# Kernel optimization log

Hardware: AMD Instinct MI355X
Metric: run time of the kernel (lower is better)

## Reference

```python
import jax, jax.numpy as jnp
import numpy as np

# Hard-coded dims from MambaLayer.__init__
D_IN = 20        # input feature dim (Dense infers it; chosen = modelInternalDim)
D_INNER = 20     # modelInternalDim
N_STATES = 10    # modelStates
DT_RANK = 5      # delta_t_rank
BATCH = 4
SEQ = 32768


def setup_inputs() -> dict:
    key = jax.random.key(0)
    ks = jax.random.split(key, 8)
    s = lambda k, shape: jax.random.normal(k, shape, dtype=jnp.float32) * 0.05
    A = jnp.tile(jnp.arange(1, N_STATES + 1, dtype=jnp.float32)[None, :], (D_INNER, 1))
    return {
        "x": jax.random.normal(ks[0], (BATCH, SEQ, D_IN), dtype=jnp.float32),
        "w_in": s(ks[1], (D_IN, 2 * D_INNER)),
        "b_in": jnp.zeros((2 * D_INNER,), jnp.float32),
        "conv_k": s(ks[2], (3, D_INNER, D_INNER)),   # (W, I, O)
        "conv_b": jnp.zeros((D_INNER,), jnp.float32),
        "w_x": s(ks[3], (D_INNER, DT_RANK + 2 * N_STATES)),
        "b_x": jnp.zeros((DT_RANK + 2 * N_STATES,), jnp.float32),
        "w_dt": s(ks[4], (DT_RANK, D_INNER)),
        "b_dt": jnp.zeros((D_INNER,), jnp.float32),
        "A_log": jnp.log(A),
        "D_param": jnp.ones((D_INNER,), jnp.float32),
    }


def _selective_scan(u, delta, A, B, C, D):
    # u, delta: (b,l,d); A: (d,n); B, C: (b,l,n); D: (d,)
    dA = jnp.einsum('bld,dn->bldn', delta, A)                  # (b,l,d,n)
    dB_u = jnp.einsum('bld,bld,bln->bldn', delta, u, B)        # (b,l,d,n)
    # tf.pad(dA[:,1:], [[0,0],[1,1],...])[:,1:] == concat(dA[:,1:], zeros) along l
    dA_shift = jnp.concatenate([dA[:, 1:], jnp.zeros_like(dA[:, :1])], axis=1)
    # reversed cumsum, exponentiate, reverse back
    dA_cumsum = jnp.exp(jnp.flip(jnp.cumsum(jnp.flip(dA_shift, axis=1), axis=1), axis=1))
    x = jnp.cumsum(dB_u * dA_cumsum, axis=1) / (dA_cumsum + 1e-12)
    y = jnp.einsum('bldn,bln->bld', x, C)
    return y + u * D


def reference(x, w_in, b_in, conv_k, conv_b, w_x, b_x, w_dt, b_dt, A_log, D_param):
    # in_projection + split (res half is unused, matching the original call())
    h = x @ w_in + b_in                                        # (b,l,2d)
    h, _res = jnp.split(h, 2, axis=-1)
    # causal Conv1D, kernel_size=3: left-pad by 2
    h = jax.lax.conv_general_dilated(
        h, conv_k, window_strides=(1,), padding=[(2, 0)],
        dimension_numbers=('NWC', 'WIO', 'NWC')) + conv_b
    h = jax.nn.silu(h)                                         # tf.nn.swish
    # ssm
    A = -jnp.exp(A_log)                                        # (d,n)
    xp = h @ w_x + b_x                                         # (b,l,r+2n)
    delta = xp[..., :DT_RANK]
    Bm = xp[..., DT_RANK:DT_RANK + N_STATES]
    Cm = xp[..., DT_RANK + N_STATES:]
    delta = jax.nn.softmax(delta @ w_dt + b_dt, axis=-1)       # (b,l,d)
    return _selective_scan(h, delta, A, Bm, Cm, D_param)
```

## Files before the change

### kernel.cpp

```cpp
#include <hip/hip_runtime.h>
#include <math.h>

#define B_   4
#define L_   32768
#define DI   20
#define NS   10
#define TBLK 128
#define NCB  256

#define OFF_AP   0u
#define OFF_RS   204800u
#define OFF_SC   409600u
#define OFF_TOT  430080u
#define OFF_H16  430192u
#define HD  0u
#define HU  2621440u
#define HB  5242880u
#define HC  6553600u

typedef _Float16 h16;
typedef _Float16 half8 __attribute__((ext_vector_type(8)));
typedef _Float16 half4 __attribute__((ext_vector_type(4)));
typedef float f32x4 __attribute__((ext_vector_type(4)));

template<int CTRL>
__device__ __forceinline__ float dppf(float idv, float src) {
    union U { float f; int i; };
    U o, s, r; o.f = idv; s.f = src;
    r.i = __builtin_amdgcn_update_dpp(o.i, s.i, CTRL, 0xf, 0xf, false);
    return r.f;
}
#define ROW_SHR1 0x111
#define ROW_SHR2 0x112
#define ROW_SHR4 0x114
#define ROW_SHR8 0x118

#define OPSCAN16(Ac, Bc) \
    { float aP = dppf<ROW_SHR1>(1.0f, Ac); float bP = dppf<ROW_SHR1>(0.0f, Bc); \
      Bc = fmaf(Ac, bP, Bc); Ac *= aP; \
      aP = dppf<ROW_SHR2>(1.0f, Ac); bP = dppf<ROW_SHR2>(0.0f, Bc); \
      Bc = fmaf(Ac, bP, Bc); Ac *= aP; \
      aP = dppf<ROW_SHR4>(1.0f, Ac); bP = dppf<ROW_SHR4>(0.0f, Bc); \
      Bc = fmaf(Ac, bP, Bc); Ac *= aP; \
      aP = dppf<ROW_SHR8>(1.0f, Ac); bP = dppf<ROW_SHR8>(0.0f, Bc); \
      Bc = fmaf(Ac, bP, Bc); Ac *= aP; }

#define SUMSCAN16(v) \
    { v += dppf<ROW_SHR1>(0.0f, v); v += dppf<ROW_SHR2>(0.0f, v); \
      v += dppf<ROW_SHR4>(0.0f, v); v += dppf<ROW_SHR8>(0.0f, v); }

#define XS_   0
#define MT_   2640
#define UL_   0
#define DS__  0
#define DUS_  2720
#define XP5_  4608
#define BS_   5448
#define WXo   6808
#define WDTo  7808
#define BDTo  7908
#define BXo   7928
#define POOLH 7956
#define WF_   7956
#define POOL2 (POOLH + 3200)

__global__ __launch_bounds__(320) void k1(
    const float* __restrict__ x,
    const float* __restrict__ w_in, const float* __restrict__ b_in,
    const float* __restrict__ conv_k, const float* __restrict__ conv_b,
    const float* __restrict__ w_x, const float* __restrict__ b_x,
    const float* __restrict__ w_dt, const float* __restrict__ b_dt,
    const float* __restrict__ A_log, const float* __restrict__ D_param,
    h16* __restrict__ dh, h16* __restrict__ uh,
    h16* __restrict__ Bh, h16* __restrict__ Ch,
    float* __restrict__ ap_ws, float* __restrict__ rs_ws, float* __restrict__ sc_ws,
    float* __restrict__ out)
{
    __shared__ __align__(16) h16 P[POOL2];
    __shared__ float beff_s[20];
    __shared__ float ALs[200];
    __shared__ float D_s[20];

    const int tid = threadIdx.x;
    const int c   = blockIdx.x;
    const int b   = blockIdx.y;
    const int l0  = c * TBLK;

    {
        float* Wf = (float*)&P[WF_];
        for (int i = tid; i < 400;  i += 320) Wf[i]       = w_in[(i/20)*40 + (i%20)];
        for (int i = tid; i < 1200; i += 320) Wf[400 + i] = conv_k[i];
        for (int i = tid; i < 200;  i += 320) ALs[i] = -__expf(A_log[i]);
        if (tid < 20) D_s[tid] = D_param[tid];
    }
    __syncthreads();

    {
        const float* Wf = (const float*)&P[WF_];
        for (int e = tid; e < 1200; e += 320) {
            int cc = e/20, o = e - cc*20;
            int w = cc/20, i = cc - w*20;
            float acc = 0.0f;
            #pragma unroll
            for (int op = 0; op < 20; op++)
                acc = fmaf(Wf[i*20 + op], Wf[400 + (w*20 + op)*20 + o], acc);
            P[MT_ + o*72 + cc] = (h16)acc;
        }
        for (int i = tid; i < 240; i += 320) {
            int o = i/12, cc = 60 + (i - (i/12)*12);
            P[MT_ + o*72 + cc] = (h16)0.0f;
        }
        for (int i = tid; i < 1000; i += 320) {
            int j = i/40, k = i - j*40;
            P[WXo + i] = (k < 20) ? (h16)w_x[k*25 + j] : (h16)0.0f;
        }
        for (int i = tid; i < 100; i += 320) P[WDTo + i] = (h16)w_dt[i];
        if (tid < 20) P[BDTo + tid] = (h16)b_dt[tid];
        if (tid < 25) P[BXo + tid] = (h16)b_x[tid];
        if (tid < 20) {
            float be = conv_b[tid];
            #pragma unroll
            for (int w = 0; w < 3; w++)
                #pragma unroll
                for (int op = 0; op < 20; op++)
                    be = fmaf(b_in[op], Wf[400 + (w*20 + op)*20 + tid], be);
            beff_s[tid] = be;
        }
        const float* xb = x + ((size_t)b*L_ + l0)*DI - 2*DI;
        for (int i = tid; i < 1320; i += 320) {
            float2 v;
            if (i >= 1300 || (c == 0 && i < 20)) v = make_float2(0.0f, 0.0f);
            else v = *(const float2*)(xb + 2*i);
            P[XS_ + 2*i]     = (h16)v.x;
            P[XS_ + 2*i + 1] = (h16)v.y;
        }
    }
    __syncthreads();

    const int wv  = tid >> 6;
    const int ln  = tid & 63;
    const int m16 = ln & 15;
    const int q   = ln >> 4;
    float uval[4][4];
    if (wv < 4) {
        #pragma unroll
        for (int jj = 0; jj < 4; jj++) {
            int job = wv*4 + jj, mt = job >> 1, nt = job & 1;
            int t_row = mt*16 + m16;
            int dcol  = nt*16 + m16;
            int dmin  = dcol < 20 ? dcol : 19;
            f32x4 acc = {0.0f, 0.0f, 0.0f, 0.0f};
            #pragma unroll
            for (int kh = 0; kh < 2; kh++) {
                half8 af, bf;
                int ab = XS_ + t_row*20 + kh*32 + (q<<3);
                *(half4*)&af         = *(const half4*)&P[ab];
                *(((half4*)&af) + 1) = *(const half4*)&P[ab + 4];
                int bb = MT_ + dmin*72 + kh*32 + (q<<3);
                *(half4*)&bf         = *(const half4*)&P[bb];
                *(((half4*)&bf) + 1) = *(const half4*)&P[bb + 4];
                acc = __builtin_amdgcn_mfma_f32_16x16x32_f16(af, bf, acc, 0, 0, 0);
            }
            float bfv = beff_s[dmin];
            #pragma unroll
            for (int r = 0; r < 4; r++) {
                float a = acc[r] + bfv;
                uval[jj][r] = a * __builtin_amdgcn_rcpf(1.0f + __expf(-a));
            }
        }
    }
    __syncthreads();

    if (wv < 4) {
        #pragma unroll
        for (int jj = 0; jj < 4; jj++) {
            int job = wv*4 + jj, mt = job >> 1, nt = job & 1;
            int dcol = nt*16 + m16;
            if (dcol < 20) {
                #pragma unroll
                for (int r = 0; r < 4; r++)
                    P[UL_ + (mt*16 + q*4 + r)*36 + dcol] = (h16)uval[jj][r];
            }
        }
    }
    __syncthreads();

    float xv[4][4];
    if (wv < 4) {
        #pragma unroll
        for (int jj = 0; jj < 4; jj++) {
            int job = wv*4 + jj, mt = job >> 1, nt = job & 1;
            int t_row = mt*16 + m16;
            int j     = nt*16 + m16;
            int jmin  = j < 25 ? j : 24;
            f32x4 acc = {0.0f, 0.0f, 0.0f, 0.0f};
            half8 af, bf;
            int ab = UL_ + t_row*36 + (q<<3);
            *(half4*)&af         = *(const half4*)&P[ab];
            *(((half4*)&af) + 1) = *(const half4*)&P[ab + 4];
            int bb = WXo + jmin*40 + (q<<3);
            *(half4*)&bf         = *(const half4*)&P[bb];
            *(((half4*)&bf) + 1) = *(const half4*)&P[bb + 4];
            acc = __builtin_amdgcn_mfma_f32_16x16x32_f16(af, bf, acc, 0, 0, 0);
            float bx = (j < 25) ? (float)P[BXo + j] : 0.0f;
            #pragma unroll
            for (int r = 0; r < 4; r++) xv[jj][r] = acc[r] + bx;
        }
        #pragma unroll
        for (int jj = 0; jj < 4; jj++) {
            int job = wv*4 + jj, mt = job >> 1, nt = job & 1;
            int j = nt*16 + m16;
            #pragma unroll
            for (int r = 0; r < 4; r++) {
                int t = mt*16 + q*4 + r;
                h16 hv = (h16)xv[jj][r];
                if (j < 5)       P[XP5_ + t*5 + j] = hv;
                else if (j < 15) P[BS_ + (j - 5)*136 + t] = hv;
                else if (j < 25) Ch[(size_t)(b*NS + (j - 15))*L_ + l0 + t] = hv;
            }
        }
    }
    __syncthreads();

    h16 urow[20];
    float dl[20];
    if (tid < 128) {
        const int t = tid;
        *(half4*)&urow[0]  = *(const half4*)&P[UL_ + t*36 + 0];
        *(half4*)&urow[4]  = *(const half4*)&P[UL_ + t*36 + 4];
        *(half4*)&urow[8]  = *(const half4*)&P[UL_ + t*36 + 8];
        *(half4*)&urow[12] = *(const half4*)&P[UL_ + t*36 + 12];
        *(half4*)&urow[16] = *(const half4*)&P[UL_ + t*36 + 16];
        #pragma unroll
        for (int d2 = 0; d2 < 20; d2++)
            uh[(size_t)(b*DI + d2)*L_ + l0 + t] = urow[d2];
        #pragma unroll
        for (int n = 0; n < NS; n++)
            Bh[(size_t)(b*NS + n)*L_ + l0 + t] = P[BS_ + n*136 + t];
        {
            float yo[20];
            #pragma unroll
            for (int d2 = 0; d2 < 20; d2++) yo[d2] = (float)urow[d2] * D_s[d2];
            float4* ob = (float4*)(out + ((size_t)b*L_ + l0 + t)*DI);
            #pragma unroll
            for (int k4 = 0; k4 < 5; k4++)
                ob[k4] = make_float4(yo[4*k4], yo[4*k4+1], yo[4*k4+2], yo[4*k4+3]);
        }
        float xq[5];
        #pragma unroll
        for (int r = 0; r < 5; r++) xq[r] = (float)P[XP5_ + t*5 + r];
        #pragma unroll
        for (int d2 = 0; d2 < 20; d2++) dl[d2] = (float)P[BDTo + d2];
        #pragma unroll
        for (int r = 0; r < 5; r++) {
            float dv = xq[r];
            #pragma unroll
            for (int d2 = 0; d2 < 20; d2++)
                dl[d2] = fmaf(dv, (float)P[WDTo + r*20 + d2], dl[d2]);
        }
        float mx = dl[0];
        #pragma unroll
        for (int d2 = 1; d2 < 20; d2++) mx = fmaxf(mx, dl[d2]);
        float sm = 0.0f;
        #pragma unroll
        for (int d2 = 0; d2 < 20; d2++) { dl[d2] = __expf(dl[d2] - mx); sm += dl[d2]; }
        float inv = __builtin_amdgcn_rcpf(sm);
        #pragma unroll
        for (int d2 = 0; d2 < 20; d2++) dl[d2] *= inv;
    }
    __syncthreads();

    if (tid < 128) {
        const int t = tid;
        #pragma unroll
        for (int d2 = 0; d2 < 20; d2++) {
            h16 dlh = (h16)dl[d2];
            P[DS__ + d2*136 + t] = dlh;
            P[DUS_ + d2*136 + t] = (h16)((float)dlh * (float)urow[d2]);
            dh[(size_t)(b*DI + d2)*L_ + l0 + t] = dlh;
        }
    }
    __syncthreads();

    const int d  = tid >> 4;
    const int s  = tid & 15;
    const int bd = b*DI + d;

    float d8[8], du8[8];
    { half8 hv = *(const half8*)&P[DS__ + d*136 + 8*s];
      #pragma unroll
      for (int j = 0; j < 8; j++) d8[j] = (float)hv[j]; }
    { half8 hv = *(const half8*)&P[DUS_ + d*136 + 8*s];
      #pragma unroll
      for (int j = 0; j < 8; j++) du8[j] = (float)hv[j]; }

    float loc8 = 0.0f;
    #pragma unroll
    for (int j = 0; j < 8; j++) loc8 += d8[j];
    float ssum = loc8;
    SUMSCAN16(ssum);
    if (s == 15) sc_ws[(size_t)bd*NCB + c] = ssum;

    float A_dn[NS];
    #pragma unroll
    for (int n = 0; n < NS; n++) A_dn[n] = ALs[d*NS + n];

    bool fastA = true;
    #pragma unroll
    for (int n = 1; n < NS; n++)
        fastA = fastA &&
            (fabsf(A_dn[n] - (float)(n+1)*A_dn[0]) <= 1e-3f*fabsf(A_dn[n]) + 1e-6f);

    float AcA[NS], BcA[NS];
    if (fastA) {
        float e1[8], ep[8];
        #pragma unroll
        for (int j = 0; j < 8; j++) { e1[j] = __expf(A_dn[0]*d8[j]); ep[j] = e1[j]; }
        #pragma unroll
        for (int n = 0; n < NS; n++) {
            half8 bv = *(const half8*)&P[BS_ + n*136 + 8*s];
            float Bc = 0.0f;
            #pragma unroll
            for (int j = 0; j < 8; j++)
                Bc = fmaf(ep[j], Bc, du8[j]*(float)bv[j]);
            BcA[n] = Bc;
            AcA[n] = __expf(A_dn[n]*loc8);
            if (n < NS-1) {
                #pragma unroll
                for (int j = 0; j < 8; j++) ep[j] *= e1[j];
            }
        }
    } else {
        #pragma unroll
        for (int n = 0; n < NS; n++) {
            half8 bv = *(const half8*)&P[BS_ + n*136 + 8*s];
            float Bc = 0.0f;
            #pragma unroll
            for (int j = 0; j < 8; j++) {
                float a = __expf(A_dn[n]*d8[j]);
                Bc = fmaf(a, Bc, du8[j]*(float)bv[j]);
            }
            BcA[n] = Bc;
            AcA[n] = __expf(A_dn[n]*loc8);
        }
    }
    #pragma unroll
    for (int n = 0; n < NS; n++) { OPSCAN16(AcA[n], BcA[n]); }
    if (s == 15) {
        const size_t o0 = ((size_t)bd*NS)*NCB + c;
        #pragma unroll
        for (int n = 0; n < NS; n++) {
            ap_ws[o0 + (size_t)n*NCB] = AcA[n];
            rs_ws[o0 + (size_t)n*NCB] = BcA[n];
        }
    }
}

__global__ __launch_bounds__(64) void kC2(
    const float* __restrict__ ap_ws, float* __restrict__ rs_ws,
    float* __restrict__ sc_ws, float* __restrict__ tot_ws)
{
    const int bd   = blockIdx.x;
    const int lane = threadIdx.x;
    const size_t sb = (size_t)bd*NCB + lane*4;

    float4 sv = *(const float4*)(sc_ws + sb);
    float l1 = sv.x, l2 = l1 + sv.y, l3 = l2 + sv.z, l4 = l3 + sv.w;
    float inc = l4;
    #pragma unroll
    for (int off = 1; off < 64; off <<= 1) {
        float t = __shfl_up(inc, off);
        if (lane >= off) inc += t;
    }
    float ex = __shfl_up(inc, 1);
    if (lane == 0) ex = 0.0f;
    *(float4*)(sc_ws + sb) = make_float4(ex, ex + l1, ex + l2, ex + l3);
    if (lane == 63) tot_ws[bd] = inc;

    #pragma unroll 2
    for (int n = 0; n < NS; n++) {
        const size_t base = ((size_t)bd*NS + n)*NCB + lane*4;
        float4 av = *(const float4*)(ap_ws + base);
        float4 rv = *(const float4*)(rs_ws + base);
        float Ac = av.x, Bc = rv.x;
        Bc = fmaf(av.y, Bc, rv.y); Ac *= av.y;
        Bc = fmaf(av.z, Bc, rv.z); Ac *= av.z;
        Bc = fmaf(av.w, Bc, rv.w); Ac *= av.w;
        #pragma unroll
        for (int off = 1; off < 64; off <<= 1) {
            float aP = __shfl_up(Ac, off);
            float bP = __shfl_up(Bc, off);
            if (lane >= off) { Bc = fmaf(Ac, bP, Bc); Ac *= aP; }
        }
        float pB = __shfl_up(Bc, 1);
        if (lane == 0) pB = 0.0f;
        float r  = pB;
        float o0 = r; r = fmaf(av.x, r, rv.x);
        float o1 = r; r = fmaf(av.y, r, rv.y);
        float o2 = r; r = fmaf(av.z, r, rv.z);
        float o3 = r;
        *(float4*)(rs_ws + base) = make_float4(o0, o1, o2, o3);
    }
}

__global__ __launch_bounds__(320) void kD(
    const h16* __restrict__ dh, const h16* __restrict__ uh,
    const h16* __restrict__ Bh, const h16* __restrict__ Ch,
    const float* __restrict__ A_log, const float* __restrict__ D_param,
    const float* __restrict__ rs_ws, const float* __restrict__ sc_ws,
    const float* __restrict__ tot_ws, float* __restrict__ out)
{
    __shared__ float ylT[20*132];
    __shared__ int anyact;
    const int tid = threadIdx.x;
    const int d   = tid >> 4;
    const int s   = tid & 15;
    const int c   = blockIdx.x;
    const int b   = blockIdx.y;
    const int bd  = b*DI + d;
    const size_t t0 = (size_t)c*TBLK + s*8;

    const float Tot = tot_ws[bd];
    float mnlog = A_log[d*NS];
    #pragma unroll
    for (int n = 1; n < NS; n++) mnlog = fminf(mnlog, A_log[d*NS + n]);
    const float Amax = -__expf(mnlog);
    const float pref_end = (c + 1 < NCB) ? sc_ws[(size_t)bd*NCB + c + 1] : Tot;
    const bool active = fmaf(Amax, Tot - pref_end, 40.0f) > 0.0f;

    if (tid == 0) anyact = 0;
    __syncthreads();
    if (active) anyact = 1;
    __syncthreads();
    if (anyact == 0) return;

    float u8[8];
    { half8 hv = *(const half8*)(uh + (size_t)bd*L_ + t0);
      #pragma unroll
      for (int j = 0; j < 8; j++) u8[j] = (float)hv[j]; }
    const float Dd = D_param[d];
    float yv[8];
    #pragma unroll
    for (int j = 0; j < 8; j++) yv[j] = u8[j]*Dd;

    if (active) {
        float A_dn[NS];
        #pragma unroll
        for (int n = 0; n < NS; n++) A_dn[n] = -__expf(A_log[d*NS + n]);
        bool fastA = true;
        #pragma unroll
        for (int n = 1; n < NS; n++)
            fastA = fastA &&
                (fabsf(A_dn[n] - (float)(n+1)*A_dn[0]) <= 1e-3f*fabsf(A_dn[n]) + 1e-6f);

        float d8[8], du8[8];
        { half8 hv = *(const half8*)(dh + (size_t)bd*L_ + t0);
          #pragma unroll
          for (int j = 0; j < 8; j++) d8[j] = (float)hv[j]; }
        #pragma unroll
        for (int j = 0; j < 8; j++) du8[j] = d8[j]*u8[j];

        float lp[8];
        { float run = 0.0f;
          #pragma unroll
          for (int j = 0; j < 8; j++) { run += d8[j]; lp[j] = run; } }
        float inc = lp[7];
        SUMSCAN16(inc);
        float ex = dppf<ROW_SHR1>(0.0f, inc);
        const float basep = sc_ws[(size_t)bd*NCB + c] + ex;

        float rin[NS];
        #pragma unroll
        for (int n = 0; n < NS; n++) rin[n] = rs_ws[((size_t)bd*NS + n)*NCB + c];

        float yacc[8];
        #pragma unroll
        for (int j = 0; j < 8; j++) yacc[j] = 0.0f;

        if (fastA) {
            float e1[8], ep[8];
            #pragma unroll
            for (int j = 0; j < 8; j++) { e1[j] = __expf(A_dn[0]*d8[j]); ep[j] = e1[j]; }
            #pragma unroll
            for (int n = 0; n < NS; n++) {
                half8 bv = *(const half8*)(Bh + (size_t)(b*NS + n)*L_ + t0);
                half8 cv = *(const half8*)(Ch + (size_t)(b*NS + n)*L_ + t0);
                float b8[8];
                #pragma unroll
                for (int j = 0; j < 8; j++) b8[j] = du8[j]*(float)bv[j];
                float Bc = 0.0f;
                #pragma unroll
                for (int j = 0; j < 8; j++) Bc = fmaf(ep[j], Bc, b8[j]);
                float Ac = __expf(A_dn[n]*lp[7]);
                OPSCAN16(Ac, Bc);
                float pA = dppf<ROW_SHR1>(1.0f, Ac);
                float pB = dppf<ROW_SHR1>(0.0f, Bc);
                float r  = fmaf(pA, rin[n], pB);

                float G[8];
                G[7] = __expf(A_dn[n]*(Tot - (basep + lp[7])));
                #pragma unroll
                for (int j = 6; j >= 0; j--) G[j] = G[j+1]*ep[j+1];
                #pragma unroll
                for (int j = 0; j < 8; j++) {
                    r = fmaf(ep[j], r, b8[j]);
                    float damp = G[j] * __builtin_amdgcn_rcpf(G[j] + 1e-12f);
                    yacc[j] = fmaf((float)cv[j]*damp, r, yacc[j]);
                }
                if (n < NS-1) {
                    #pragma unroll
                    for (int j = 0; j < 8; j++) ep[j] *= e1[j];
                }
            }
        } else {
            #pragma unroll 2
            for (int n = 0; n < NS; n++) {
                half8 bv = *(const half8*)(Bh + (size_t)(b*NS + n)*L_ + t0);
                half8 cv = *(const half8*)(Ch + (size_t)(b*NS + n)*L_ + t0);
                float a8[8], b8[8];
                #pragma unroll
                for (int j = 0; j < 8; j++) {
                    a8[j] = __expf(A_dn[n]*d8[j]);
                    b8[j] = du8[j]*(float)bv[j];
                }
                float Bc = 0.0f;
                #pragma unroll
                for (int j = 0; j < 8; j++) Bc = fmaf(a8[j], Bc, b8[j]);
                float Ac = __expf(A_dn[n]*lp[7]);
                OPSCAN16(Ac, Bc);
                float pA = dppf<ROW_SHR1>(1.0f, Ac);
                float pB = dppf<ROW_SHR1>(0.0f, Bc);
                float r  = fmaf(pA, rin[n], pB);

                float G[8];
                G[7] = __expf(A_dn[n]*(Tot - (basep + lp[7])));
                #pragma unroll
                for (int j = 6; j >= 0; j--) G[j] = G[j+1]*a8[j+1];
                #pragma unroll
                for (int j = 0; j < 8; j++) {
                    r = fmaf(a8[j], r, b8[j]);
                    float damp = G[j] * __builtin_amdgcn_rcpf(G[j] + 1e-12f);
                    yacc[j] = fmaf((float)cv[j]*damp, r, yacc[j]);
                }
            }
        }
        #pragma unroll
        for (int j = 0; j < 8; j++) yv[j] = fmaf(u8[j], Dd, yacc[j]);
    }

    *(float4*)&ylT[d*132 + 8*s]     = *(float4*)(yv);
    *(float4*)&ylT[d*132 + 8*s + 4] = *(float4*)(yv + 4);
    __syncthreads();

    float4* ob4 = (float4*)(out + ((size_t)b*L_ + (size_t)c*TBLK)*DI);
    for (int i = tid; i < TBLK*DI/4; i += 320) {
        int t = i / 5, qq = (i - t*5)*4;
        ob4[i] = make_float4(ylT[qq*132 + t], ylT[(qq+1)*132 + t],
                             ylT[(qq+2)*132 + t], ylT[(qq+3)*132 + t]);
    }
}

extern "C" void kernel_launch(void* const* d_in, const int* in_sizes, int n_in,
                              void* d_out, int out_size, void* d_ws, size_t ws_size,
                              hipStream_t stream) {
    const float* x      = (const float*)d_in[0];
    const float* w_in   = (const float*)d_in[1];
    const float* b_in   = (const float*)d_in[2];
    const float* conv_k = (const float*)d_in[3];
    const float* conv_b = (const float*)d_in[4];
    const float* w_x    = (const float*)d_in[5];
    const float* b_x    = (const float*)d_in[6];
    const float* w_dt   = (const float*)d_in[7];
    const float* b_dt   = (const float*)d_in[8];
    const float* A_log  = (const float*)d_in[9];
    const float* D_par  = (const float*)d_in[10];
    float* out = (float*)d_out;
    float* ws  = (float*)d_ws;

    float* ap_ws  = ws + OFF_AP;
    float* rs_ws  = ws + OFF_RS;
    float* sc_ws  = ws + OFF_SC;
    float* tot_ws = ws + OFF_TOT;
    h16*   hbase  = (h16*)(ws + OFF_H16);
    h16* dh  = hbase + HD;
    h16* uh  = hbase + HU;
    h16* Bh  = hbase + HB;
    h16* Ch  = hbase + HC;

    k1<<<dim3(NCB, B_), 320, 0, stream>>>(x, w_in, b_in, conv_k, conv_b,
                                          w_x, b_x, w_dt, b_dt, A_log, D_par,
                                          dh, uh, Bh, Ch,
                                          ap_ws, rs_ws, sc_ws, out);
    kC2<<<B_*DI, 64, 0, stream>>>(ap_ws, rs_ws, sc_ws, tot_ws);
    kD<<<dim3(NCB, B_), 320, 0, stream>>>(dh, uh, Bh, Ch, A_log, D_par,
                                          rs_ws, sc_ws, tot_ws, out);
}
```

Baseline: 117.1 us.

## Fold chunk-carry scan kernel into final kernel, recomputing prefixes per block

Removes the separate kC2 launch that scanned the per-chunk totals and state carries. Each kD block now rereads all 256 chunk summaries for its channel and, with 16 lanes per channel, does a masked reduction and operator scan to get its own prefix total and incoming state. This drops a launch and a device-wide dependency step. In exchange every block does redundant work, roughly quadratic in the chunk count overall, and rereads the ap/rs workspace.

```diff
diff --git a/kernel.cpp b/kernel.cpp
--- a/kernel.cpp
+++ b/kernel.cpp
@@ -11,7 +11,6 @@
 #define OFF_AP   0u
 #define OFF_RS   204800u
 #define OFF_SC   409600u
-#define OFF_TOT  430080u
 #define OFF_H16  430192u
 #define HD  0u
 #define HU  2621440u
@@ -356,76 +355,47 @@
     }
 }
 
-__global__ __launch_bounds__(64) void kC2(
-    const float* __restrict__ ap_ws, float* __restrict__ rs_ws,
-    float* __restrict__ sc_ws, float* __restrict__ tot_ws)
-{
-    const int bd   = blockIdx.x;
-    const int lane = threadIdx.x;
-    const size_t sb = (size_t)bd*NCB + lane*4;
-
-    float4 sv = *(const float4*)(sc_ws + sb);
-    float l1 = sv.x, l2 = l1 + sv.y, l3 = l2 + sv.z, l4 = l3 + sv.w;
-    float inc = l4;
-    #pragma unroll
-    for (int off = 1; off < 64; off <<= 1) {
-        float t = __shfl_up(inc, off);
-        if (lane >= off) inc += t;
-    }
-    float ex = __shfl_up(inc, 1);
-    if (lane == 0) ex = 0.0f;
-    *(float4*)(sc_ws + sb) = make_float4(ex, ex + l1, ex + l2, ex + l3);
-    if (lane == 63) tot_ws[bd] = inc;
-
-    #pragma unroll 2
-    for (int n = 0; n < NS; n++) {
-        const size_t base = ((size_t)bd*NS + n)*NCB + lane*4;
-        float4 av = *(const float4*)(ap_ws + base);
-        float4 rv = *(const float4*)(rs_ws + base);
-        float Ac = av.x, Bc = rv.x;
-        Bc = fmaf(av.y, Bc, rv.y); Ac *= av.y;
-        Bc = fmaf(av.z, Bc, rv.z); Ac *= av.z;
-        Bc = fmaf(av.w, Bc, rv.w); Ac *= av.w;
-        #pragma unroll
-        for (int off = 1; off < 64; off <<= 1) {
-            float aP = __shfl_up(Ac, off);
-            float bP = __shfl_up(Bc, off);
-            if (lane >= off) { Bc = fmaf(Ac, bP, Bc); Ac *= aP; }
-        }
-        float pB = __shfl_up(Bc, 1);
-        if (lane == 0) pB = 0.0f;
-        float r  = pB;
-        float o0 = r; r = fmaf(av.x, r, rv.x);
-        float o1 = r; r = fmaf(av.y, r, rv.y);
-        float o2 = r; r = fmaf(av.z, r, rv.z);
-        float o3 = r;
-        *(float4*)(rs_ws + base) = make_float4(o0, o1, o2, o3);
-    }
-}
-
 __global__ __launch_bounds__(320) void kD(
     const h16* __restrict__ dh, const h16* __restrict__ uh,
     const h16* __restrict__ Bh, const h16* __restrict__ Ch,
     const float* __restrict__ A_log, const float* __restrict__ D_param,
-    const float* __restrict__ rs_ws, const float* __restrict__ sc_ws,
-    const float* __restrict__ tot_ws, float* __restrict__ out)
+    const float* __restrict__ ap_ws, const float* __restrict__ rs_ws,
+    const float* __restrict__ sc_ws, float* __restrict__ out)
 {
     __shared__ float ylT[20*132];
     __shared__ int anyact;
     const int tid = threadIdx.x;
     const int d   = tid >> 4;
     const int s   = tid & 15;
+    const int lnw = tid & 63;
     const int c   = blockIdx.x;
     const int b   = blockIdx.y;
     const int bd  = b*DI + d;
     const size_t t0 = (size_t)c*TBLK + s*8;
 
-    const float Tot = tot_ws[bd];
+    float totp = 0.0f, clipp = 0.0f;
+    {
+        const float4* sc4 = (const float4*)(sc_ws + (size_t)bd*NCB + s*16);
+        #pragma unroll
+        for (int q4 = 0; q4 < 4; q4++) {
+            float4 v = sc4[q4];
+            int base = s*16 + q4*4;
+            totp  += v.x + v.y + v.z + v.w;
+            clipp += (base + 0 < c ? v.x : 0.0f) + (base + 1 < c ? v.y : 0.0f)
+                   + (base + 2 < c ? v.z : 0.0f) + (base + 3 < c ? v.w : 0.0f);
+        }
+    }
+    SUMSCAN16(totp);
+    SUMSCAN16(clipp);
+    const float Tot = __shfl(totp,  lnw | 15);
+    const float Pc  = __shfl(clipp, lnw | 15);
+    const float sc_c = sc_ws[(size_t)bd*NCB + c];
+    const float pref_end = Pc + sc_c;
+
     float mnlog = A_log[d*NS];
     #pragma unroll
     for (int n = 1; n < NS; n++) mnlog = fminf(mnlog, A_log[d*NS + n]);
     const float Amax = -__expf(mnlog);
-    const float pref_end = (c + 1 < NCB) ? sc_ws[(size_t)bd*NCB + c + 1] : Tot;
     const bool active = fmaf(Amax, Tot - pref_end, 40.0f) > 0.0f;
 
     if (tid == 0) anyact = 0;
@@ -453,6 +423,26 @@
             fastA = fastA &&
                 (fabsf(A_dn[n] - (float)(n+1)*A_dn[0]) <= 1e-3f*fabsf(A_dn[n]) + 1e-6f);
 
+        float rin[NS];
+        #pragma unroll
+        for (int n = 0; n < NS; n++) {
+            const float4* ap4 = (const float4*)(ap_ws + ((size_t)bd*NS + n)*NCB + s*16);
+            const float4* rs4 = (const float4*)(rs_ws + ((size_t)bd*NS + n)*NCB + s*16);
+            float Aa = 1.0f, Bb = 0.0f;
+            #pragma unroll
+            for (int k4 = 0; k4 < 4; k4++) {
+                float4 av = ap4[k4];
+                float4 rv = rs4[k4];
+                int base = s*16 + k4*4;
+                if (base + 0 < c) { Bb = fmaf(av.x, Bb, rv.x); Aa *= av.x; }
+                if (base + 1 < c) { Bb = fmaf(av.y, Bb, rv.y); Aa *= av.y; }
+                if (base + 2 < c) { Bb = fmaf(av.z, Bb, rv.z); Aa *= av.z; }
+                if (base + 3 < c) { Bb = fmaf(av.w, Bb, rv.w); Aa *= av.w; }
+            }
+            OPSCAN16(Aa, Bb);
+            rin[n] = __shfl(Bb, lnw | 15);
+        }
+
         float d8[8], du8[8];
         { half8 hv = *(const half8*)(dh + (size_t)bd*L_ + t0);
           #pragma unroll
@@ -467,11 +457,7 @@
         float inc = lp[7];
         SUMSCAN16(inc);
         float ex = dppf<ROW_SHR1>(0.0f, inc);
-        const float basep = sc_ws[(size_t)bd*NCB + c] + ex;
-
-        float rin[NS];
-        #pragma unroll
-        for (int n = 0; n < NS; n++) rin[n] = rs_ws[((size_t)bd*NS + n)*NCB + c];
+        const float basep = Pc + ex;
 
         float yacc[8];
         #pragma unroll
@@ -580,7 +566,6 @@
     float* ap_ws  = ws + OFF_AP;
     float* rs_ws  = ws + OFF_RS;
     float* sc_ws  = ws + OFF_SC;
-    float* tot_ws = ws + OFF_TOT;
     h16*   hbase  = (h16*)(ws + OFF_H16);
     h16* dh  = hbase + HD;
     h16* uh  = hbase + HU;
@@ -591,7 +576,6 @@
                                           w_x, b_x, w_dt, b_dt, A_log, D_par,
                                           dh, uh, Bh, Ch,
                                           ap_ws, rs_ws, sc_ws, out);
-    kC2<<<B_*DI, 64, 0, stream>>>(ap_ws, rs_ws, sc_ws, tot_ws);
     kD<<<dim3(NCB, B_), 320, 0, stream>>>(dh, uh, Bh, Ch, A_log, D_par,
-                                          rs_ws, sc_ws, tot_ws, out);
+                                          ap_ws, rs_ws, sc_ws, out);
 }
```

After: 130.1 us. +11.1%, slower.
